# Kernel tuning notes

Hardware: AMD Instinct MI355X
Metric: run time of the kernel (lower is better)

## Reference

```python
import jax, jax.numpy as jnp
import numpy as np

N = 100000; E = 1600000; IN = 64; H = 128; G = 64

def setup_inputs() -> dict:
    key = jax.random.key(0)
    ks = jax.random.split(key, 8)
    h = jax.random.normal(ks[0], (N, IN), jnp.float32)
    src = jax.random.randint(ks[1], (E,), 0, N, jnp.int32)
    dst = jax.random.randint(ks[2], (E,), 0, N, jnp.int32)
    graph_ids = jnp.sort(jax.random.randint(ks[3], (N,), 0, G, jnp.int32))
    W1 = jax.random.normal(ks[4], (IN, H), jnp.float32) / jnp.sqrt(IN)
    b1 = jnp.zeros((H,), jnp.float32)
    W2 = jax.random.normal(ks[5], (H, H), jnp.float32) / jnp.sqrt(H)
    b2 = jnp.zeros((H,), jnp.float32)
    Wr = jax.random.normal(ks[6], (H, 1), jnp.float32) / jnp.sqrt(H)
    br = jnp.zeros((1,), jnp.float32)
    return {"h": h, "src": src, "dst": dst, "graph_ids": graph_ids, "num_graphs": G,
            "W1": W1, "b1": b1, "W2": W2, "b2": b2, "Wr": Wr, "br": br}

def _gcn(x, src, dst, inv_sqrt_out, inv_sqrt_in, W, b):
    # DGL GraphConv, norm='both', aggregate-first (in_feats <= out_feats):
    # out = D_in^{-1/2} * A * (D_out^{-1/2} * x) @ W + b
    x = x * inv_sqrt_out[:, None]
    agg = jax.ops.segment_sum(x[src], dst, num_segments=x.shape[0])  # [N, d]
    return agg @ W * inv_sqrt_in[:, None] + b

def reference(h, src, dst, graph_ids, num_graphs, W1, b1, W2, b2, Wr, br):
    n = h.shape[0]
    ones_e = jnp.ones(src.shape[0], h.dtype)
    deg_out = jnp.maximum(jax.ops.segment_sum(ones_e, src, num_segments=n), 1.0)
    deg_in = jnp.maximum(jax.ops.segment_sum(ones_e, dst, num_segments=n), 1.0)
    iso = jax.lax.rsqrt(deg_out)
    isi = jax.lax.rsqrt(deg_in)
    h1 = jax.nn.relu(_gcn(h, src, dst, iso, isi, W1, b1))   # conv1 has activation=relu
    h2 = _gcn(h1, src, dst, iso, isi, W2, b2)               # conv2 has no activation
    hf = jax.nn.relu(h2)                                    # outer F.relu in forward
    # mean_nodes: per-graph mean readout
    sums = jax.ops.segment_sum(hf, graph_ids, num_segments=num_graphs)  # [G, H]
    cnt = jnp.maximum(jax.ops.segment_sum(jnp.ones(n, hf.dtype), graph_ids, num_segments=num_graphs), 1.0)
    hg = sums / cnt[:, None]
    return hg @ Wr + br  # [G, 1]
```

## Files before the change

kernel.cpp:

```cpp
#include <hip/hip_runtime.h>

#define N_IN 64
#define N_H  128
#define N_G  64
#define HP   4
#define HC   64
#define YSTRIDE 132

#define SWZB(r) (((r) & 7) << 3)

typedef unsigned int   uint32;
typedef unsigned short ushort16;
typedef unsigned char  uchar8;
typedef float floatx2 __attribute__((ext_vector_type(2)));
typedef short bf16x8 __attribute__((ext_vector_type(8)));
typedef float f32x4  __attribute__((ext_vector_type(4)));

#define FP8_SCALE    32.0f
#define FP8_INVSCALE 0.03125f

#if defined(__has_builtin)
#if __has_builtin(__builtin_amdgcn_cvt_pk_f32_fp8) && __has_builtin(__builtin_amdgcn_cvt_pk_fp8_f32)
#define HW_FP8 1
#endif
#endif

__device__ __forceinline__ float bf2f(ushort16 u) {
    union { uint32 i; float f; } x; x.i = ((uint32)u) << 16; return x.f;
}
__device__ __forceinline__ ushort16 f2bf(float f) {
    union { float f; uint32 i; } x; x.f = f;
    uint32 r = x.i + 0x7FFFu + ((x.i >> 16) & 1u);
    return (ushort16)(r >> 16);
}

#ifndef HW_FP8
__device__ __forceinline__ uint32 f2e4m3(float x) {
    union { float f; uint32 i; } v; v.f = x;
    uint32 s = (v.i >> 24) & 0x80u;
    uint32 a = v.i & 0x7FFFFFFFu;
    if (a < 0x3C000000u) return s;
    uint32 r = a + 0x0007FFFFu + ((a >> 20) & 1u);
    int e = (int)(r >> 23) - 120;
    if (e <= 0) return s;
    if (e > 15) return s | 0x7Eu;
    return s | ((uint32)e << 3) | ((r >> 20) & 7u);
}
__device__ __forceinline__ floatx2 e4m3pair(uint32 u) {
    floatx2 o;
    #pragma unroll
    for (int k = 0; k < 2; ++k) {
        uint32 b = (u >> (8 * k)) & 0xFFu;
        uint32 m = b & 0x7Fu;
        union { uint32 i; float f; } x;
        x.i = ((b & 0x80u) << 24) | ((m << 20) + 0x3C000000u);
        o[k] = m ? x.f : 0.f;
    }
    return o;
}
#endif

__device__ __forceinline__ uint32 pack4fp8(float o0, float o1, float o2, float o3) {
#ifdef HW_FP8
    int r = __builtin_amdgcn_cvt_pk_fp8_f32(o0, o1, 0, false);
    r     = __builtin_amdgcn_cvt_pk_fp8_f32(o2, o3, r, true);
    return (uint32)r;
#else
    return f2e4m3(o0) | (f2e4m3(o1) << 8) | (f2e4m3(o2) << 16) | (f2e4m3(o3) << 24);
#endif
}


__global__ __launch_bounds__(1024) void hist_kernel(const int* __restrict__ src,
        const int* __restrict__ dst, ushort16* __restrict__ part_cnt,
        int N, int E, int npp, int ec) {
    extern __shared__ int cnt[];
    int p = blockIdx.x & (HP - 1);
    int c = blockIdx.x >> 2;
    int nlo = p * npp;
    int nhi = min(nlo + npp, N);
    int nn = nhi - nlo;
    if (nn <= 0) return;
    int tid = threadIdx.x;
    for (int i = tid; i < nn; i += 1024) cnt[i] = 0;
    __syncthreads();
    int elo = c * ec, ehi = min(elo + ec, E);
    for (int e = elo + tid; e < ehi; e += 1024) {
        int s = src[e];
        unsigned so = (unsigned)(s - nlo);
        if (so < (unsigned)nn) atomicAdd(&cnt[so], 1);
        int d = dst[e];
        unsigned dof = (unsigned)(d - nlo);
        if (dof < (unsigned)nn) atomicAdd(&cnt[dof], 1 << 16);
    }
    __syncthreads();
    for (int i = tid; i < nn; i += 1024) {
        int v = cnt[i];
        part_cnt[(size_t)c * N + nlo + i] =
            (ushort16)((v & 0xFF) | ((v >> 8) & 0xFF00));
    }
}

__global__ void reduce_norm_kernel(const ushort16* __restrict__ part_cnt,
        uchar8* __restrict__ pre, const int* __restrict__ gid,
        float* __restrict__ iso, float* __restrict__ isi, int* __restrict__ deg_in,
        int* __restrict__ gstart, int* __restrict__ gend, int N) {
    int n = blockIdx.x * blockDim.x + threadIdx.x;
    if (n >= N) return;
    int so = 0, si = 0;
    #pragma unroll
    for (int c = 0; c < HC; ++c) {
        int v = part_cnt[(size_t)c * N + n];
        so += v & 0xFF;
        pre[(size_t)c * N + n] = (uchar8)si;
        si += v >> 8;
    }
    iso[n] = rsqrtf((float)max(so, 1));
    isi[n] = rsqrtf((float)max(si, 1));
    deg_in[n] = si;
    int g = gid[n];
    if (n == 0 || gid[n - 1] != g) gstart[g] = n;
    if (n == N - 1 || gid[n + 1] != g) gend[g] = n + 1;
}

__global__ __launch_bounds__(1024) void scan_partial(const int* __restrict__ deg_in,
                                                     int* __restrict__ bsum, int N) {
    int i = blockIdx.x * 1024 + threadIdx.x;
    int v = (i < N) ? deg_in[i] : 0;
    int lane = threadIdx.x & 63, wv = threadIdx.x >> 6;
    int s = v;
    #pragma unroll
    for (int off = 1; off < 64; off <<= 1) s += __shfl_xor(s, off);
    __shared__ int ws[16];
    if (lane == 0) ws[wv] = s;
    __syncthreads();
    if (threadIdx.x == 0) {
        int t = 0;
        #pragma unroll
        for (int k = 0; k < 16; ++k) t += ws[k];
        bsum[blockIdx.x] = t;
    }
}

__global__ void scan_bsum(int* __restrict__ bsum, int nb) {
    int tid = threadIdx.x;
    int lane = tid & 63, wv = tid >> 6;
    int v = (tid < nb) ? bsum[tid] : 0;
    int s = v;
    #pragma unroll
    for (int off = 1; off < 64; off <<= 1) {
        int t = __shfl_up(s, off);
        if (lane >= off) s += t;
    }
    __shared__ int w0tot;
    if (wv == 0 && lane == 63) w0tot = s;
    __syncthreads();
    if (wv == 1) s += w0tot;
    if (tid < nb) bsum[tid] = s - v;
}

__global__ __launch_bounds__(1024) void scan_write(const int* __restrict__ deg_in,
                                                   const int* __restrict__ bsum,
                                                   int* __restrict__ row_ptr, int N) {
    int i = blockIdx.x * 1024 + threadIdx.x;
    int v = (i < N) ? deg_in[i] : 0;
    int lane = threadIdx.x & 63, wv = threadIdx.x >> 6;
    int s = v;
    #pragma unroll
    for (int off = 1; off < 64; off <<= 1) {
        int t = __shfl_up(s, off);
        if (lane >= off) s += t;
    }
    __shared__ int ws[16];
    if (lane == 63) ws[wv] = s;
    __syncthreads();
    if (wv == 0 && lane < 16) {
        int x = ws[lane];
        int s2 = x;
        #pragma unroll
        for (int off = 1; off < 16; off <<= 1) {
            int t = __shfl_up(s2, off);
            if (lane >= off) s2 += t;
        }
        ws[lane] = s2;
    }
    __syncthreads();
    int base = bsum[blockIdx.x] + (wv > 0 ? ws[wv - 1] : 0);
    if (i < N) row_ptr[i] = base + s - v;
    if (i == N - 1) row_ptr[N] = base + s;
}

__global__ __launch_bounds__(1024) void fill_kernel(const int* __restrict__ src,
        const int* __restrict__ dst, const int* __restrict__ row_ptr,
        const uchar8* __restrict__ pre, int* __restrict__ col,
        int N, int E, int npp, int ec) {
    extern __shared__ int cur[];
    int p = blockIdx.x & (HP - 1);
    int c = blockIdx.x >> 2;
    int nlo = p * npp;
    int nhi = min(nlo + npp, N);
    int nn = nhi - nlo;
    if (nn <= 0) return;
    int tid = threadIdx.x;
    for (int i = tid; i < nn; i += 1024)
        cur[i] = row_ptr[nlo + i] + (int)pre[(size_t)c * N + nlo + i];
    __syncthreads();
    int elo = c * ec, ehi = min(elo + ec, E);
    for (int e = elo + tid; e < ehi; e += 1024) {
        int d = dst[e];
        unsigned off = (unsigned)(d - nlo);
        if (off < (unsigned)nn) {
            int slot = atomicAdd(&cur[off], 1);
            col[slot] = src[e];
        }
    }
}

__global__ __launch_bounds__(256) void scale_h_kernel(const float* __restrict__ h,
        const float* __restrict__ iso, ushort16* __restrict__ hs, int N) {
    int t = blockIdx.x * 256 + threadIdx.x;
    int base = t * 8;
    if (base >= N * N_IN) return;
    int n = base >> 6;
    float s = iso[n];
    float4 a = *(const float4*)&h[base];
    float4 b = *(const float4*)&h[base + 4];
    uint4 pk;
    pk.x = (uint32)f2bf(a.x * s) | ((uint32)f2bf(a.y * s) << 16);
    pk.y = (uint32)f2bf(a.z * s) | ((uint32)f2bf(a.w * s) << 16);
    pk.z = (uint32)f2bf(b.x * s) | ((uint32)f2bf(b.y * s) << 16);
    pk.w = (uint32)f2bf(b.z * s) | ((uint32)f2bf(b.w * s) << 16);
    *(uint4*)&hs[base] = pk;
}

__global__ __launch_bounds__(1024) void wprep_kernel(const float* __restrict__ W1,
        const float* __restrict__ W2, ushort16* __restrict__ W1T,
        ushort16* __restrict__ W2T) {
    int t = blockIdx.x * 1024 + threadIdx.x;
    if (t < 128 * 128) {
        int j = t >> 7, k = t & 127;
        W2T[j * 128 + k] = f2bf(W2[k * 128 + j]);
    } else if (t < 128 * 128 + 128 * 64) {
        int q = t - 128 * 128;
        int j = q >> 6, k = q & 63;
        W1T[j * 64 + k] = f2bf(W1[k * 128 + j]);
    }
}


__global__ __launch_bounds__(256) void gather1_kernel(const ushort16* __restrict__ hs,
        const int* __restrict__ row_ptr, const int* __restrict__ col,
        ushort16* __restrict__ agg1bf, int N) {
    int wave = __builtin_amdgcn_readfirstlane(threadIdx.x >> 6);
    int lane = threadIdx.x & 63;
    int n = blockIdx.x * 4 + wave;
    if (n >= N) return;
    int p0 = row_ptr[n], p1 = row_ptr[n + 1];
    float acc = 0.f;
    for (int pb = p0; pb < p1; pb += 64) {
        int cnt = min(64, p1 - pb);
        int cv = col[min(pb + lane, p1 - 1)];
        for (int i0 = 0; i0 < cnt; i0 += 16) {
            int   sidx[16];
            float w[16];
            #pragma unroll
            for (int i = 0; i < 16; ++i) {
                int q = i0 + i;
                sidx[i] = __shfl(cv, min(q, cnt - 1));
                w[i] = (q < cnt) ? 1.f : 0.f;
            }
            float v[16];
            #pragma unroll
            for (int i = 0; i < 16; ++i)
                v[i] = bf2f(hs[(size_t)sidx[i] * N_IN + lane]);
            #pragma unroll
            for (int i = 0; i < 16; ++i)
                acc = fmaf(v[i], w[i], acc);
        }
    }
    agg1bf[(size_t)n * N_IN + lane] = f2bf(acc);
}

__global__ __launch_bounds__(256) void gather2_kernel(const ushort16* __restrict__ h18,
        const int* __restrict__ row_ptr, const int* __restrict__ col,
        uint32* __restrict__ agg2bf, int N) {
    int wave = __builtin_amdgcn_readfirstlane(threadIdx.x >> 6);
    int lane = threadIdx.x & 63;
    int n = blockIdx.x * 4 + wave;
    if (n >= N) return;
    int p0 = row_ptr[n], p1 = row_ptr[n + 1];
    float ax = 0.f, ay = 0.f;
    for (int pb = p0; pb < p1; pb += 64) {
        int cnt = min(64, p1 - pb);
        int cv = col[min(pb + lane, p1 - 1)];
        for (int i0 = 0; i0 < cnt; i0 += 16) {
            int   sidx[16];
            float w[16];
            #pragma unroll
            for (int i = 0; i < 16; ++i) {
                int q = i0 + i;
                sidx[i] = __shfl(cv, min(q, cnt - 1));
                w[i] = (q < cnt) ? FP8_INVSCALE : 0.f;
            }
            uint32 u[16];
            #pragma unroll
            for (int i = 0; i < 16; ++i)
                u[i] = h18[(size_t)sidx[i] * 64 + lane];
            #pragma unroll
            for (int i = 0; i < 16; ++i) {
#ifdef HW_FP8
                floatx2 d = __builtin_amdgcn_cvt_pk_f32_fp8((int)u[i], false);
#else
                floatx2 d = e4m3pair(u[i]);
#endif
                ax = fmaf(d.x, w[i], ax);
                ay = fmaf(d.y, w[i], ay);
            }
        }
    }
    agg2bf[(size_t)n * 64 + lane] = (uint32)f2bf(ax) | ((uint32)f2bf(ay) << 16);
}

__global__ __launch_bounds__(512) void mm1_kernel(const ushort16* __restrict__ agg1bf,
        const ushort16* __restrict__ W1T, const float* __restrict__ b1,
        const float* __restrict__ isi, const float* __restrict__ iso,
        uchar8* __restrict__ h18, int N) {
    __shared__ union {
        struct { ushort16 A[128 * 64]; ushort16 W[128 * 64]; } st;
        float Y[128 * YSTRIDE];
    } u;
    __shared__ float ISI[128], ISO[128];
    int t = threadIdx.x;
    int n0 = blockIdx.x * 128;
    {
        int r = t >> 2;
        int k0 = (t & 3) * 16;
        bool valid = (n0 + r) < N;
        const uint4* ga = (const uint4*)(agg1bf + (size_t)(n0 + r) * 64 + k0);
        const uint4* gw = (const uint4*)(W1T + (size_t)r * 64 + k0);
        #pragma unroll
        for (int q = 0; q < 2; ++q) {
            uint4 va = valid ? ga[q] : uint4{0, 0, 0, 0};
            uint4 vw = gw[q];
            int kg = k0 + q * 8;
            *(uint4*)&u.st.A[r * 64 + (kg ^ SWZB(r))] = va;
            *(uint4*)&u.st.W[r * 64 + (kg ^ SWZB(r))] = vw;
        }
        if (t < 128) {
            ISI[t] = (n0 + t < N) ? isi[n0 + t] : 0.f;
            ISO[t] = (n0 + t < N) ? iso[n0 + t] * FP8_SCALE : 0.f;
        }
    }
    __syncthreads();
    int w = __builtin_amdgcn_readfirstlane(t >> 6);
    int l = t & 63, l15 = l & 15, lhi = l >> 4;
    int jcol = w * 16 + l15;
    float b1j = b1[jcol];
    f32x4 acc[8] = {};
    #pragma unroll
    for (int kk = 0; kk < 2; ++kk) {
        int kb = kk * 32 + lhi * 8;
        bf16x8 bf = *(bf16x8*)&u.st.W[jcol * 64 + (kb ^ SWZB(jcol))];
        #pragma unroll
        for (int tm = 0; tm < 8; ++tm) {
            int row = tm * 16 + l15;
            bf16x8 af = *(bf16x8*)&u.st.A[row * 64 + (kb ^ SWZB(row))];
            acc[tm] = __builtin_amdgcn_mfma_f32_16x16x32_bf16(af, bf, acc[tm], 0, 0, 0);
        }
    }
    __syncthreads();
    #pragma unroll
    for (int tm = 0; tm < 8; ++tm) {
        #pragma unroll
        for (int i = 0; i < 4; ++i) {
            int m = tm * 16 + lhi * 4 + i;
            u.Y[m * YSTRIDE + jcol] =
                fmaxf(fmaf(acc[tm][i], ISI[m], b1j), 0.f) * ISO[m];
        }
    }
    __syncthreads();
    {
        int r = t >> 2;
        int c0 = (t & 3) * 32;
        if (n0 + r < N) {
            uint32 b[8];
            #pragma unroll
            for (int q = 0; q < 8; ++q) {
                float4 y4 = *(float4*)&u.Y[r * YSTRIDE + c0 + q * 4];
                b[q] = pack4fp8(y4.x, y4.y, y4.z, y4.w);
            }
            uchar8* dstp = h18 + (size_t)(n0 + r) * 128 + c0;
            *(uint4*)dstp        = uint4{b[0], b[1], b[2], b[3]};
            *(uint4*)(dstp + 16) = uint4{b[4], b[5], b[6], b[7]};
        }
    }
}

__global__ __launch_bounds__(512) void mm2_kernel(const uint32* __restrict__ agg2bf,
        const ushort16* __restrict__ W2T, const float* __restrict__ b2,
        const float* __restrict__ isi, const int* __restrict__ gid,
        float* __restrict__ sums, int N) {
    __shared__ union {
        struct { ushort16 A[128 * 128]; ushort16 W[128 * 128]; } st;
        float Y[128 * YSTRIDE];
    } u;
    __shared__ float ISI[128];
    int t = threadIdx.x;
    int n0 = blockIdx.x * 128;
    {
        int r = t >> 2;
        int k0 = (t & 3) * 32;
        bool valid = (n0 + r) < N;
        const uint4* ga = (const uint4*)((const ushort16*)agg2bf + (size_t)(n0 + r) * 128 + k0);
        const uint4* gw = (const uint4*)(W2T + (size_t)r * 128 + k0);
        #pragma unroll
        for (int q = 0; q < 4; ++q) {
            uint4 va = valid ? ga[q] : uint4{0, 0, 0, 0};
            uint4 vw = gw[q];
            int kg = k0 + q * 8;
            *(uint4*)&u.st.A[r * 128 + (kg ^ SWZB(r))] = va;
            *(uint4*)&u.st.W[r * 128 + (kg ^ SWZB(r))] = vw;
        }
        if (t < 128) ISI[t] = (n0 + t < N) ? isi[n0 + t] : 0.f;
    }
    __syncthreads();
    int w = __builtin_amdgcn_readfirstlane(t >> 6);
    int l = t & 63, l15 = l & 15, lhi = l >> 4;
    int jcol = w * 16 + l15;
    float b2j = b2[jcol];
    f32x4 acc[8] = {};
    #pragma unroll
    for (int kk = 0; kk < 4; ++kk) {
        int kb = kk * 32 + lhi * 8;
        bf16x8 bf = *(bf16x8*)&u.st.W[jcol * 128 + (kb ^ SWZB(jcol))];
        #pragma unroll
        for (int tm = 0; tm < 8; ++tm) {
            int row = tm * 16 + l15;
            bf16x8 af = *(bf16x8*)&u.st.A[row * 128 + (kb ^ SWZB(row))];
            acc[tm] = __builtin_amdgcn_mfma_f32_16x16x32_bf16(af, bf, acc[tm], 0, 0, 0);
        }
    }
    __syncthreads();
    #pragma unroll
    for (int tm = 0; tm < 8; ++tm) {
        #pragma unroll
        for (int i = 0; i < 4; ++i) {
            int m = tm * 16 + lhi * 4 + i;
            u.Y[m * YSTRIDE + jcol] = fmaxf(fmaf(acc[tm][i], ISI[m], b2j), 0.f);
        }
    }
    __syncthreads();
    int j = t & 127;
    int seg = t >> 7;
    float racc = 0.f;
    int cur = -1;
    for (int i = 0; i < 32; ++i) {
        int ln = seg * 32 + i;
        int n = n0 + ln;
        if (n >= N) break;
        float y = u.Y[ln * YSTRIDE + j];
        int g = gid[n];
        if (g != cur) {
            if (cur >= 0) atomicAdd(&sums[cur * N_H + j], racc);
            racc = 0.f;
            cur = g;
        }
        racc += y;
    }
    if (cur >= 0) atomicAdd(&sums[cur * N_H + j], racc);
}

__global__ void out_kernel(const float* __restrict__ sums, const int* __restrict__ gstart,
                           const int* __restrict__ gend, const float* __restrict__ Wr,
                           const float* __restrict__ br, float* __restrict__ out) {
    int g = blockIdx.x;
    int j = threadIdx.x;
    float c = fmaxf((float)(gend[g] - gstart[g]), 1.f);
    float v = sums[g * N_H + j] / c * Wr[j];
    for (int off = 32; off > 0; off >>= 1) v += __shfl_down(v, off);
    __shared__ float part[2];
    if ((threadIdx.x & 63) == 0) part[threadIdx.x >> 6] = v;
    __syncthreads();
    if (threadIdx.x == 0) out[g] = part[0] + part[1] + br[0];
}

static inline size_t align_up(size_t x, size_t a) { return (x + a - 1) & ~(a - 1); }

extern "C" void kernel_launch(void* const* d_in, const int* in_sizes, int n_in,
                              void* d_out, int out_size, void* d_ws, size_t ws_size,
                              hipStream_t stream) {
    const float* h  = (const float*)d_in[0];
    const int* src  = (const int*)d_in[1];
    const int* dst  = (const int*)d_in[2];
    const int* gid  = (const int*)d_in[3];
    const float* W1 = (const float*)d_in[5];
    const float* b1 = (const float*)d_in[6];
    const float* W2 = (const float*)d_in[7];
    const float* b2 = (const float*)d_in[8];
    const float* Wr = (const float*)d_in[9];
    const float* br = (const float*)d_in[10];
    float* out = (float*)d_out;

    int N = in_sizes[0] / N_IN;
    int E = in_sizes[1];
    int nb  = (N + 1023) / 1024;
    int npp = (N + HP - 1) / HP;
    int ec  = (E + HC - 1) / HC;
    size_t hist_lds = (size_t)npp * 4;

    char* ws = (char*)d_ws;
    size_t off = 0;
    auto alloc = [&](size_t bytes) -> char* {
        char* p = ws + off;
        off = align_up(off + bytes, 256);
        return p;
    };
    int*   gstart  = (int*)alloc((size_t)N_G * 4);
    int*   gend    = (int*)alloc((size_t)N_G * 4);
    float* sums    = (float*)alloc((size_t)N_G * N_H * 4);
    size_t zero_bytes = off;
    int*      deg_in  = (int*)alloc((size_t)N * 4);
    float*    iso     = (float*)alloc((size_t)N * 4);
    float*    isi     = (float*)alloc((size_t)N * 4);
    int*      row_ptr = (int*)alloc((size_t)(N + 1) * 4);
    int*      bsum    = (int*)alloc((size_t)128 * 4);
    int*      col     = (int*)alloc((size_t)E * 4);
    ushort16* hs      = (ushort16*)alloc((size_t)N * N_IN * 2);
    uchar8*   h18     = (uchar8*)alloc((size_t)N * N_H);
    ushort16* W1T     = (ushort16*)alloc((size_t)128 * 64 * 2);
    ushort16* W2T     = (ushort16*)alloc((size_t)128 * 128 * 2);
    ushort16* agg1bf  = (ushort16*)alloc((size_t)N * N_IN * 2);
    uint32*   agg2bf  = (uint32*)alloc((size_t)N * 64 * 4);
    ushort16* part_cnt = (ushort16*)agg1bf;
    uchar8*   pre      = (uchar8*)agg2bf;

    hipMemsetAsync(d_ws, 0, zero_bytes, stream);

    wprep_kernel<<<24, 1024, 0, stream>>>(W1, W2, W1T, W2T);
    hist_kernel<<<HP * HC, 1024, hist_lds, stream>>>(src, dst, part_cnt, N, E, npp, ec);
    reduce_norm_kernel<<<(N + 255) / 256, 256, 0, stream>>>(part_cnt, pre, gid, iso, isi,
                                                            deg_in, gstart, gend, N);
    scan_partial<<<nb, 1024, 0, stream>>>(deg_in, bsum, N);
    scan_bsum<<<1, 128, 0, stream>>>(bsum, nb);
    scan_write<<<nb, 1024, 0, stream>>>(deg_in, bsum, row_ptr, N);
    fill_kernel<<<HP * HC, 1024, hist_lds, stream>>>(src, dst, row_ptr, pre, col, N, E, npp, ec);
    scale_h_kernel<<<(N * N_IN / 8 + 255) / 256, 256, 0, stream>>>(h, iso, hs, N);

    gather1_kernel<<<(N + 3) / 4, 256, 0, stream>>>(hs, row_ptr, col, agg1bf, N);
    mm1_kernel<<<(N + 127) / 128, 512, 0, stream>>>(agg1bf, W1T, b1, isi, iso, h18, N);
    gather2_kernel<<<(N + 3) / 4, 256, 0, stream>>>((const ushort16*)h18, row_ptr, col, agg2bf, N);
    mm2_kernel<<<(N + 127) / 128, 512, 0, stream>>>(agg2bf, W2T, b2, isi, gid, sums, N);
    out_kernel<<<N_G, N_H, 0, stream>>>(sums, gstart, gend, Wr, br, out);
}
```

Baseline: 211.6 us.

## Split gather waves into two half-wave edge streams with wider per-lane loads

Both gather kernels now have each half of the wavefront handle alternating edges. Each lane loads a 4-byte word, which holds two bf16 or four fp8 features, instead of a 2-byte or 2-element load. The halves then combine their partial sums with a cross-lane shuffle and only the lower half writes. This halves the number of gather load instructions per edge and widens each access, aiming to reduce per-edge memory-instruction and latency overhead in the bandwidth-bound neighbor aggregation. The cost is an extra shuffle-reduction, idle lanes on the store, and possible wasted slots when a node's edge count is odd or small.

```diff
diff --git a/kernel.cpp b/kernel.cpp
--- a/kernel.cpp
+++ b/kernel.cpp
@@ -46,11 +46,12 @@
     if (e > 15) return s | 0x7Eu;
     return s | ((uint32)e << 3) | ((r >> 20) & 7u);
 }
-__device__ __forceinline__ floatx2 e4m3pair(uint32 u) {
+__device__ __forceinline__ floatx2 e4m3word(uint32 u, bool hi) {
     floatx2 o;
+    uint32 w = hi ? (u >> 16) : u;
     #pragma unroll
     for (int k = 0; k < 2; ++k) {
-        uint32 b = (u >> (8 * k)) & 0xFFu;
+        uint32 b = (w >> (8 * k)) & 0xFFu;
         uint32 m = b & 0x7Fu;
         union { uint32 i; float f; } x;
         x.i = ((b & 0x80u) << 24) | ((m << 20) + 0x3C000000u);
@@ -248,77 +249,99 @@
 }
 
 
-__global__ __launch_bounds__(256) void gather1_kernel(const ushort16* __restrict__ hs,
+__global__ __launch_bounds__(256) void gather1_kernel(const uint32* __restrict__ hsw,
         const int* __restrict__ row_ptr, const int* __restrict__ col,
-        ushort16* __restrict__ agg1bf, int N) {
+        uint32* __restrict__ agg1w, int N) {
     int wave = __builtin_amdgcn_readfirstlane(threadIdx.x >> 6);
     int lane = threadIdx.x & 63;
+    int half = lane >> 5, l32 = lane & 31;
     int n = blockIdx.x * 4 + wave;
     if (n >= N) return;
     int p0 = row_ptr[n], p1 = row_ptr[n + 1];
-    float acc = 0.f;
+    float a0 = 0.f, a1 = 0.f;
     for (int pb = p0; pb < p1; pb += 64) {
         int cnt = min(64, p1 - pb);
         int cv = col[min(pb + lane, p1 - 1)];
         for (int i0 = 0; i0 < cnt; i0 += 16) {
-            int   sidx[16];
-            float w[16];
-            #pragma unroll
-            for (int i = 0; i < 16; ++i) {
-                int q = i0 + i;
+            int   sidx[8];
+            float w[8];
+            #pragma unroll
+            for (int i = 0; i < 8; ++i) {
+                int q = i0 + 2 * i + half;
                 sidx[i] = __shfl(cv, min(q, cnt - 1));
                 w[i] = (q < cnt) ? 1.f : 0.f;
             }
-            float v[16];
-            #pragma unroll
-            for (int i = 0; i < 16; ++i)
-                v[i] = bf2f(hs[(size_t)sidx[i] * N_IN + lane]);
-            #pragma unroll
-            for (int i = 0; i < 16; ++i)
-                acc = fmaf(v[i], w[i], acc);
-        }
-    }
-    agg1bf[(size_t)n * N_IN + lane] = f2bf(acc);
-}
-
-__global__ __launch_bounds__(256) void gather2_kernel(const ushort16* __restrict__ h18,
+            uint32 u[8];
+            #pragma unroll
+            for (int i = 0; i < 8; ++i)
+                u[i] = hsw[(size_t)sidx[i] * 32 + l32];
+            #pragma unroll
+            for (int i = 0; i < 8; ++i) {
+                union { uint32 i; float f; } lo, hi;
+                lo.i = u[i] << 16;
+                hi.i = u[i] & 0xFFFF0000u;
+                a0 = fmaf(lo.f, w[i], a0);
+                a1 = fmaf(hi.f, w[i], a1);
+            }
+        }
+    }
+    a0 += __shfl_xor(a0, 32);
+    a1 += __shfl_xor(a1, 32);
+    if (half == 0)
+        agg1w[(size_t)n * 32 + l32] = (uint32)f2bf(a0) | ((uint32)f2bf(a1) << 16);
+}
+
+__global__ __launch_bounds__(256) void gather2_kernel(const uint32* __restrict__ h18w,
         const int* __restrict__ row_ptr, const int* __restrict__ col,
-        uint32* __restrict__ agg2bf, int N) {
+        uint32* __restrict__ agg2w, int N) {
     int wave = __builtin_amdgcn_readfirstlane(threadIdx.x >> 6);
     int lane = threadIdx.x & 63;
+    int half = lane >> 5, l32 = lane & 31;
     int n = blockIdx.x * 4 + wave;
     if (n >= N) return;
     int p0 = row_ptr[n], p1 = row_ptr[n + 1];
-    float ax = 0.f, ay = 0.f;
+    float a0 = 0.f, a1 = 0.f, a2 = 0.f, a3 = 0.f;
     for (int pb = p0; pb < p1; pb += 64) {
         int cnt = min(64, p1 - pb);
         int cv = col[min(pb + lane, p1 - 1)];
         for (int i0 = 0; i0 < cnt; i0 += 16) {
-            int   sidx[16];
-            float w[16];
-            #pragma unroll
-            for (int i = 0; i < 16; ++i) {
-                int q = i0 + i;
+            int   sidx[8];
+            float w[8];
+            #pragma unroll
+            for (int i = 0; i < 8; ++i) {
+                int q = i0 + 2 * i + half;
                 sidx[i] = __shfl(cv, min(q, cnt - 1));
                 w[i] = (q < cnt) ? FP8_INVSCALE : 0.f;
             }
-            uint32 u[16];
-            #pragma unroll
-            for (int i = 0; i < 16; ++i)
-                u[i] = h18[(size_t)sidx[i] * 64 + lane];
-            #pragma unroll
-            for (int i = 0; i < 16; ++i) {
+            uint32 u[8];
+            #pragma unroll
+            for (int i = 0; i < 8; ++i)
+                u[i] = h18w[(size_t)sidx[i] * 32 + l32];
+            #pragma unroll
+            for (int i = 0; i < 8; ++i) {
 #ifdef HW_FP8
-                floatx2 d = __builtin_amdgcn_cvt_pk_f32_fp8((int)u[i], false);
+                floatx2 dlo = __builtin_amdgcn_cvt_pk_f32_fp8((int)u[i], false);
+                floatx2 dhi = __builtin_amdgcn_cvt_pk_f32_fp8((int)u[i], true);
 #else
-                floatx2 d = e4m3pair(u[i]);
+                floatx2 dlo = e4m3word(u[i], false);
+                floatx2 dhi = e4m3word(u[i], true);
 #endif
-                ax = fmaf(d.x, w[i], ax);
-                ay = fmaf(d.y, w[i], ay);
+                a0 = fmaf(dlo.x, w[i], a0);
+                a1 = fmaf(dlo.y, w[i], a1);
+                a2 = fmaf(dhi.x, w[i], a2);
+                a3 = fmaf(dhi.y, w[i], a3);
             }
         }
     }
-    agg2bf[(size_t)n * 64 + lane] = (uint32)f2bf(ax) | ((uint32)f2bf(ay) << 16);
+    a0 += __shfl_xor(a0, 32);
+    a1 += __shfl_xor(a1, 32);
+    a2 += __shfl_xor(a2, 32);
+    a3 += __shfl_xor(a3, 32);
+    if (half == 0) {
+        uint32 w0 = (uint32)f2bf(a0) | ((uint32)f2bf(a1) << 16);
+        uint32 w1 = (uint32)f2bf(a2) | ((uint32)f2bf(a3) << 16);
+        *(uint2*)&agg2w[(size_t)n * 64 + l32 * 2] = uint2{w0, w1};
+    }
 }
 
 __global__ __launch_bounds__(512) void mm1_kernel(const ushort16* __restrict__ agg1bf,
@@ -546,9 +569,11 @@
     fill_kernel<<<HP * HC, 1024, hist_lds, stream>>>(src, dst, row_ptr, pre, col, N, E, npp, ec);
     scale_h_kernel<<<(N * N_IN / 8 + 255) / 256, 256, 0, stream>>>(h, iso, hs, N);
 
-    gather1_kernel<<<(N + 3) / 4, 256, 0, stream>>>(hs, row_ptr, col, agg1bf, N);
+    gather1_kernel<<<(N + 3) / 4, 256, 0, stream>>>((const uint32*)hs, row_ptr, col,
+                                                    (uint32*)agg1bf, N);
     mm1_kernel<<<(N + 127) / 128, 512, 0, stream>>>(agg1bf, W1T, b1, isi, iso, h18, N);
-    gather2_kernel<<<(N + 3) / 4, 256, 0, stream>>>((const ushort16*)h18, row_ptr, col, agg2bf, N);
+    gather2_kernel<<<(N + 3) / 4, 256, 0, stream>>>((const uint32*)h18, row_ptr, col,
+                                                    agg2bf, N);
     mm2_kernel<<<(N + 127) / 128, 512, 0, stream>>>(agg2bf, W2T, b2, isi, gid, sums, N);
     out_kernel<<<N_G, N_H, 0, stream>>>(sums, gstart, gend, Wr, br, out);
 }
```

Result: faster. 202.1 us (-4.5%).
